# Kernel optimization log

Measured on AMD Instinct MI355X. Metric: run time of the kernel, lower is better.

Reference implementation:

```python
import jax, jax.numpy as jnp
import numpy as np

BSZ, L, D_Q, S_Q = 2, 2048, 512, 4
EPS = 1e-6


def quat_mul(a, b):
    ar, ai, aj, ak = a[..., 0], a[..., 1], a[..., 2], a[..., 3]
    br, bi, bj, bk = b[..., 0], b[..., 1], b[..., 2], b[..., 3]
    return jnp.stack((
        ar * br - ai * bi - aj * bj - ak * bk,
        ar * bi + ai * br + aj * bk - ak * bj,
        ar * bj - ai * bk + aj * br + ak * bi,
        ar * bk + ai * bj - aj * bi + ak * br,
    ), axis=-1)


def quat_inv(q):
    r, i, j, k = q[..., 0], q[..., 1], q[..., 2], q[..., 3]
    s = 1.0 / (r * r + i * i + j * j + k * k + EPS)
    return jnp.stack((r * s, -i * s, -j * s, -k * s), axis=-1)


def setup_inputs() -> dict:
    key = jax.random.key(0)
    ks = jax.random.split(key, 8)
    u = jax.random.normal(ks[0], (BSZ, L, D_Q, 4), dtype=jnp.float32)
    dt = jax.random.uniform(ks[1], (BSZ, L, D_Q), dtype=jnp.float32)
    B_in = jax.random.normal(ks[2], (BSZ, L, S_Q, 4), dtype=jnp.float32)
    C_in = jax.random.normal(ks[3], (BSZ, L, S_Q, 4), dtype=jnp.float32)
    # A_log init: log(arange(1, S_q+1)) repeated over D_q rows
    A_log = jnp.tile(jnp.log(jnp.arange(1, S_Q + 1, dtype=jnp.float32)), (D_Q, 1))
    A_i = jax.random.normal(ks[4], (D_Q, S_Q), dtype=jnp.float32) * 0.01
    A_j = jax.random.normal(ks[5], (D_Q, S_Q), dtype=jnp.float32) * 0.01
    A_k = jax.random.normal(ks[6], (D_Q, S_Q), dtype=jnp.float32) * 0.01
    return {"u": u, "dt": dt, "B_in": B_in, "C_in": C_in,
            "A_log": A_log, "A_i": A_i, "A_j": A_j, "A_k": A_k}


def reference(u, dt, B_in, C_in, A_log, A_i, A_j, A_k):
    # A quaternion: real part -exp(A_log), imaginary parts A_i/j/k  [D_q, S_q, 4]
    A_quat = jnp.stack([-jnp.exp(A_log), A_i, A_j, A_k], axis=-1)
    dt_b = dt[..., None, None]                      # [B, L, D_q, 1, 1]
    z = dt_b * A_quat                               # [B, L, D_q, S_q, 4]
    one = jnp.zeros_like(z).at[..., 0].set(1.0)     # quaternion identity
    num = one + 0.5 * z
    den = one - 0.5 * z
    den_inv = quat_inv(den)
    q = quat_mul(den_inv, num)                      # Cayley transition [B,L,D_q,S_q,4]
    dB = quat_mul(den_inv * dt_b, B_in[:, :, None])  # [B,L,D_q,S_q,4]
    Bu = quat_mul(dB, u[:, :, :, None])             # [B,L,D_q,S_q,4]

    def step(h, qb):
        qt, but = qb
        h = quat_mul(qt, h) + but
        return h, h

    h0 = jnp.zeros((u.shape[0], u.shape[2], A_quat.shape[1], 4), u.dtype)
    _, h_all = jax.lax.scan(step, h0, (jnp.swapaxes(q, 0, 1), jnp.swapaxes(Bu, 0, 1)))
    h_all = jnp.swapaxes(h_all, 0, 1)               # [B, L, D_q, S_q, 4]
    yh = quat_mul(C_in[:, :, None], h_all)
    return yh.sum(axis=3)                           # [B, L, D_q, 4]
```

## Files before the change

### kernel.cpp

```cpp
#include <hip/hip_runtime.h>

#define BSZ   2
#define LSEQ  2048
#define DQ    512
#define SQ    4
#define EPSQ  1e-6f

typedef float nfloat4 __attribute__((ext_vector_type(4)));
typedef float nfloat2 __attribute__((ext_vector_type(2)));

__device__ __forceinline__ nfloat2 mk2(float x, float y) { nfloat2 v; v.x = x; v.y = y; return v; }

struct PQuat { nfloat2 ri, jk; };

__device__ __forceinline__ PQuat pq_of(const float4 v) {
    PQuat p; p.ri = mk2(v.x, v.y); p.jk = mk2(v.z, v.w); return p;
}
__device__ __forceinline__ float4 f4_of(const PQuat p) {
    return make_float4(p.ri.x, p.ri.y, p.jk.x, p.jk.y);
}

__device__ __forceinline__ PQuat pqmul(const PQuat a, const PQuat b) {
    const float ar = a.ri.x, ai = a.ri.y, aj = a.jk.x, ak = a.jk.y;
    PQuat o;
    o.ri = ar*b.ri + ai*mk2(-b.ri.y,  b.ri.x)
         + aj*mk2(-b.jk.x,  b.jk.y) + ak*mk2(-b.jk.y, -b.jk.x);
    o.jk = ar*b.jk + ai*mk2(-b.jk.y,  b.jk.x)
         + aj*mk2( b.ri.x, -b.ri.y) + ak*mk2( b.ri.y,  b.ri.x);
    return o;
}

__device__ __forceinline__ PQuat pqmuladd(const PQuat a, const PQuat b, const PQuat c) {
    const float ar = a.ri.x, ai = a.ri.y, aj = a.jk.x, ak = a.jk.y;
    PQuat o;
    o.ri = c.ri + ar*b.ri + ai*mk2(-b.ri.y,  b.ri.x)
         + aj*mk2(-b.jk.x,  b.jk.y) + ak*mk2(-b.jk.y, -b.jk.x);
    o.jk = c.jk + ar*b.jk + ai*mk2(-b.jk.y,  b.jk.x)
         + aj*mk2( b.ri.x, -b.ri.y) + ak*mk2( b.ri.y,  b.ri.x);
    return o;
}

struct HA { float r, i; nfloat2 jk; float p2, n2r; };

__device__ __forceinline__ HA load_hA(const float* __restrict__ Alog,
                                      const float* __restrict__ Ai,
                                      const float* __restrict__ Aj,
                                      const float* __restrict__ Ak, int idx) {
    HA h;
    h.r  = -0.5f * __expf(Alog[idx]);
    h.i  =  0.5f * Ai[idx];
    h.jk = mk2(0.5f * Aj[idx], 0.5f * Ak[idx]);
    h.p2 = h.r*h.r + h.i*h.i + h.jk.x*h.jk.x + h.jk.y*h.jk.y;
    h.n2r = -2.0f * h.r;
    return h;
}

__device__ __forceinline__ void cayley_pk(const float a, const float aa, const HA& hA,
                                          const PQuat B, const PQuat U,
                                          PQuat& q, PQuat& Bu) {
    const float dd = __builtin_fmaf(aa, hA.p2, __builtin_fmaf(a, hA.n2r, 1.0f + EPSQ));
    const float sv = __builtin_amdgcn_rcpf(dd);
    const float nr = __builtin_fmaf(-aa, hA.p2, 1.0f);
    const float as = a * sv;
    const float s2a = as + as;
    q.ri = mk2(nr * sv, s2a * hA.i);
    q.jk = s2a * hA.jk;
    PQuat cd;
    cd.ri = mk2(__builtin_fmaf(-a, hA.r, 1.0f), a * hA.i);
    cd.jk = a * hA.jk;
    const PQuat cb = pqmul(cd, B);
    PQuat dB; dB.ri = as * cb.ri; dB.jk = as * cb.jk;
    Bu = pqmul(dB, U);
}

struct Quat { float r, i, j, k; };
__device__ __forceinline__ Quat qmul(const Quat a, const Quat b) {
    Quat o;
    o.r = a.r*b.r - a.i*b.i - a.j*b.j - a.k*b.k;
    o.i = a.r*b.i + a.i*b.r + a.j*b.k - a.k*b.j;
    o.j = a.r*b.j - a.i*b.k + a.j*b.r + a.k*b.i;
    o.k = a.r*b.k + a.i*b.j - a.j*b.i + a.k*b.r;
    return o;
}
__device__ __forceinline__ Quat qmuladd(const Quat a, const Quat b, const Quat c) {
    Quat o;
    o.r = c.r + a.r*b.r - a.i*b.i - a.j*b.j - a.k*b.k;
    o.i = c.i + a.r*b.i + a.i*b.r + a.j*b.k - a.k*b.j;
    o.j = c.j + a.r*b.j - a.i*b.k + a.j*b.r + a.k*b.i;
    o.k = c.k + a.r*b.k + a.i*b.j - a.j*b.i + a.k*b.r;
    return o;
}
__device__ __forceinline__ Quat q_of(const float4 v) { return Quat{v.x, v.y, v.z, v.w}; }
__device__ __forceinline__ float4 f4s_of(const Quat q) { return make_float4(q.r, q.i, q.j, q.k); }

template<int NCH>
__global__ __launch_bounds__(256, 6) void qssm_pass1(
    const float* __restrict__ u, const float* __restrict__ dt,
    const float* __restrict__ Bin,
    const float* __restrict__ Alog, const float* __restrict__ Ai,
    const float* __restrict__ Aj,   const float* __restrict__ Ak,
    float4* __restrict__ WQ, float4* __restrict__ WB)
{
    constexpr int CH = LSEQ / NCH;
    const int t  = threadIdx.x;
    const int dl = t & 127;
    const int sh = t >> 7;
    const int d  = blockIdx.x * 128 + dl;
    const int c  = blockIdx.y;
    const int b  = blockIdx.z;
    const int s0 = sh * 2;
    const int t0 = c * CH;

    HA hA[2];
    hA[0] = load_hA(Alog, Ai, Aj, Ak, d*SQ + s0);
    hA[1] = load_hA(Alog, Ai, Aj, Ak, d*SQ + s0 + 1);

    const int base = (b*LSEQ + t0);
    const float*  dtp = dt + (size_t)base*DQ + d;
    const float4* up  = (const float4*)u   + (size_t)base*DQ + d;
    const float4* Bp  = (const float4*)Bin + (size_t)base*SQ + s0;

    PQuat Q[2], Bc[2];
    {
        const float a  = *dtp;
        const float aa = a * a;
        const PQuat U  = pq_of(*up);
#pragma unroll
        for (int ss = 0; ss < 2; ++ss) {
            PQuat q, Bu;
            cayley_pk(a, aa, hA[ss], pq_of(Bp[ss]), U, q, Bu);
            Q[ss] = q; Bc[ss] = Bu;
        }
        dtp += DQ; up += DQ; Bp += SQ;
    }
#pragma unroll 2
    for (int j = 1; j < CH; ++j) {
        const float a  = *dtp;
        const float aa = a * a;
        const PQuat U  = pq_of(*up);
#pragma unroll
        for (int ss = 0; ss < 2; ++ss) {
            PQuat q, Bu;
            cayley_pk(a, aa, hA[ss], pq_of(Bp[ss]), U, q, Bu);
            Bc[ss] = pqmuladd(q, Bc[ss], Bu);
            Q[ss]  = pqmul(q, Q[ss]);
        }
        dtp += DQ; up += DQ; Bp += SQ;
    }
#pragma unroll
    for (int ss = 0; ss < 2; ++ss) {
        const size_t idx = ((size_t)(b*SQ + s0 + ss)*NCH + c)*DQ + d;
        WQ[idx] = f4_of(Q[ss]);
        WB[idx] = f4_of(Bc[ss]);
    }
}

template<int NCH>
__global__ __launch_bounds__(512) void qssm_pass2(
    const float4* __restrict__ WQ, float4* __restrict__ WB)
{
    constexpr int GS = 8;
    constexpr int NG = NCH / GS;
    __shared__ float4 QL[NG][16];
    __shared__ float4 BL[NG][16];
    __shared__ float4 HS[NG][16];

    const int t  = threadIdx.x;
    const int i  = t & 15;
    const int g  = t >> 4;
    const int bs = blockIdx.x >> 5;
    const int d  = (blockIdx.x & 31) * 16 + i;
    const size_t chbase = (size_t)bs * NCH * DQ + d;

    size_t idx = chbase + (size_t)(g * GS) * DQ;
    Quat Qa = q_of(WQ[idx]);
    Quat Ba = q_of(WB[idx]);
#pragma unroll
    for (int j = 1; j < GS; ++j) {
        idx += DQ;
        const Quat Qc = q_of(WQ[idx]);
        const Quat Bc = q_of(WB[idx]);
        Ba = qmuladd(Qc, Ba, Bc);
        Qa = qmul(Qc, Qa);
    }
    QL[g][i] = f4s_of(Qa);
    BL[g][i] = f4s_of(Ba);
    __syncthreads();

    if (t < 16) {
        Quat h{0.f, 0.f, 0.f, 0.f};
#pragma unroll
        for (int gg = 0; gg < NG; ++gg) {
            HS[gg][t] = f4s_of(h);
            h = qmuladd(q_of(QL[gg][t]), h, q_of(BL[gg][t]));
        }
    }
    __syncthreads();

    Quat h = q_of(HS[g][i]);
    idx = chbase + (size_t)(g * GS) * DQ;
#pragma unroll
    for (int j = 0; j < GS; ++j) {
        const Quat Qc = q_of(WQ[idx]);
        const Quat Bc = q_of(WB[idx]);
        WB[idx] = f4s_of(h);
        h = qmuladd(Qc, h, Bc);
        idx += DQ;
    }
}

template<int NCH>
__global__ __launch_bounds__(256, 6) void qssm_pass3(
    const float* __restrict__ u, const float* __restrict__ dt,
    const float* __restrict__ Bin, const float* __restrict__ Cin,
    const float* __restrict__ Alog, const float* __restrict__ Ai,
    const float* __restrict__ Aj,   const float* __restrict__ Ak,
    const float4* __restrict__ WB, float* __restrict__ out)
{
    constexpr int CH = LSEQ / NCH;
    const int t    = threadIdx.x;
    const int lane = t & 63;
    const int wv   = t >> 6;
    const int dl   = lane & 31;
    const int sh   = lane >> 5;
    const int s0   = sh * 2;
    const int d = blockIdx.x * 128 + wv * 32 + dl;
    const int c = blockIdx.y;
    const int b = blockIdx.z;
    const int t0 = c * CH;

    HA hA[2];
    PQuat h[2];
#pragma unroll
    for (int ss = 0; ss < 2; ++ss) {
        hA[ss] = load_hA(Alog, Ai, Aj, Ak, d*SQ + s0 + ss);
        h[ss] = pq_of(WB[((size_t)(b*SQ + s0 + ss)*NCH + c)*DQ + d]);
    }
    const int base = (b*LSEQ + t0);
    const float*  dtp  = dt + (size_t)base*DQ + d;
    const float4* up   = (const float4*)u   + (size_t)base*DQ + d;
    const float4* Bp   = (const float4*)Bin + (size_t)base*SQ + s0;
    const float4* Cp   = (const float4*)Cin + (size_t)base*SQ + s0;
    nfloat4*      outp = (nfloat4*)out + (size_t)base*DQ + d;

#pragma unroll 2
    for (int j = 0; j < CH; ++j) {
        const float a  = *dtp;
        const float aa = a * a;
        const PQuat U  = pq_of(*up);
        PQuat y; y.ri = mk2(0.f, 0.f); y.jk = mk2(0.f, 0.f);
#pragma unroll
        for (int ss = 0; ss < 2; ++ss) {
            const PQuat Cq = pq_of(Cp[ss]);
            PQuat q, Bu;
            cayley_pk(a, aa, hA[ss], pq_of(Bp[ss]), U, q, Bu);
            h[ss] = pqmuladd(q, h[ss], Bu);
            y = pqmuladd(Cq, h[ss], y);
        }
        float yr = y.ri.x + __shfl_xor(y.ri.x, 32);
        float yi = y.ri.y + __shfl_xor(y.ri.y, 32);
        float yj = y.jk.x + __shfl_xor(y.jk.x, 32);
        float yk = y.jk.y + __shfl_xor(y.jk.y, 32);
        if (sh == 0) {
            const nfloat4 yv = {yr, yi, yj, yk};
            __builtin_nontemporal_store(yv, outp);
        }
        dtp += DQ; up += DQ; Bp += SQ; Cp += SQ; outp += DQ;
    }
}

template<int NCH>
static void launch_all(const float* u, const float* dt, const float* Bin,
                       const float* Cin, const float* Alog, const float* Ai,
                       const float* Aj, const float* Ak,
                       float* out, void* d_ws, hipStream_t stream) {
    const size_t elems = (size_t)BSZ * SQ * NCH * DQ;
    float4* WQ = (float4*)d_ws;
    float4* WB = WQ + elems;
    dim3 g1(DQ / 128, NCH, BSZ);
    qssm_pass1<NCH><<<g1, 256, 0, stream>>>(u, dt, Bin, Alog, Ai, Aj, Ak, WQ, WB);
    qssm_pass2<NCH><<<(BSZ*SQ*DQ)/16, 16*(NCH/8), 0, stream>>>(WQ, WB);
    dim3 g3(DQ / 128, NCH, BSZ);
    qssm_pass3<NCH><<<g3, 256, 0, stream>>>(u, dt, Bin, Cin, Alog, Ai, Aj, Ak, WB, out);
}

extern "C" void kernel_launch(void* const* d_in, const int* in_sizes, int n_in,
                              void* d_out, int out_size, void* d_ws, size_t ws_size,
                              hipStream_t stream) {
    const float* u    = (const float*)d_in[0];
    const float* dt   = (const float*)d_in[1];
    const float* Bin  = (const float*)d_in[2];
    const float* Cin  = (const float*)d_in[3];
    const float* Alog = (const float*)d_in[4];
    const float* Ai   = (const float*)d_in[5];
    const float* Aj   = (const float*)d_in[6];
    const float* Ak   = (const float*)d_in[7];
    float* out = (float*)d_out;

    auto ws_need = [](int nch) -> size_t {
        return 2ull * BSZ * SQ * (size_t)nch * DQ * sizeof(float4);
    };
    if (ws_size >= ws_need(256)) {
        launch_all<256>(u, dt, Bin, Cin, Alog, Ai, Aj, Ak, out, d_ws, stream);
    } else if (ws_size >= ws_need(128)) {
        launch_all<128>(u, dt, Bin, Cin, Alog, Ai, Aj, Ak, out, d_ws, stream);
    } else {
        launch_all<64>(u, dt, Bin, Cin, Alog, Ai, Aj, Ak, out, d_ws, stream);
    }
}
```

Before: 156.1 us.

## Fuse three scan passes into one cooperative kernel with grid syncs

```diff
diff --git a/kernel.cpp b/kernel.cpp
--- a/kernel.cpp
+++ b/kernel.cpp
@@ -1,4 +1,7 @@
 #include <hip/hip_runtime.h>
+#include <hip/hip_cooperative_groups.h>
+
+namespace cg = cooperative_groups;
 
 #define BSZ   2
 #define LSEQ  2048
@@ -92,6 +95,188 @@
 }
 __device__ __forceinline__ Quat q_of(const float4 v) { return Quat{v.x, v.y, v.z, v.w}; }
 __device__ __forceinline__ float4 f4s_of(const Quat q) { return make_float4(q.r, q.i, q.j, q.k); }
+
+template<int NCH>
+__global__ __launch_bounds__(256, 4) void qssm_fused(
+    const float* __restrict__ u, const float* __restrict__ dt,
+    const float* __restrict__ Bin, const float* __restrict__ Cin,
+    const float* __restrict__ Alog, const float* __restrict__ Ai,
+    const float* __restrict__ Aj,   const float* __restrict__ Ak,
+    float4* __restrict__ WQ, float4* __restrict__ WB, float* __restrict__ out)
+{
+    constexpr int CH  = LSEQ / NCH;
+    constexpr int NDB = DQ / 128;
+    constexpr int NT  = BSZ * NCH * NDB;
+    constexpr int NUNITS = (BSZ * SQ) * (DQ / 16);
+    constexpr int GS  = NCH / 16;
+
+    __shared__ float4 QL[16][16];
+    __shared__ float4 BL[16][16];
+    __shared__ float4 HS[16][16];
+
+    const int t = threadIdx.x;
+    cg::grid_group grid = cg::this_grid();
+
+    {
+        const int dl = t & 127;
+        const int sh = t >> 7;
+        const int s0 = sh * 2;
+        for (int tid = blockIdx.x; tid < NT; tid += gridDim.x) {
+            const int dblk = tid % NDB;
+            const int c    = (tid / NDB) % NCH;
+            const int b    =  tid / (NDB * NCH);
+            const int d    = dblk * 128 + dl;
+            const int t0   = c * CH;
+
+            HA hA0 = load_hA(Alog, Ai, Aj, Ak, d*SQ + s0);
+            HA hA1 = load_hA(Alog, Ai, Aj, Ak, d*SQ + s0 + 1);
+
+            const int base = (b*LSEQ + t0);
+            const float*  dtp = dt + (size_t)base*DQ + d;
+            const float4* up  = (const float4*)u   + (size_t)base*DQ + d;
+            const float4* Bp  = (const float4*)Bin + (size_t)base*SQ + s0;
+
+            PQuat Q[2], Bc[2];
+            {
+                const float a  = *dtp;
+                const float aa = a * a;
+                const PQuat U  = pq_of(*up);
+                PQuat q, Bu;
+                cayley_pk(a, aa, hA0, pq_of(Bp[0]), U, q, Bu);
+                Q[0] = q; Bc[0] = Bu;
+                cayley_pk(a, aa, hA1, pq_of(Bp[1]), U, q, Bu);
+                Q[1] = q; Bc[1] = Bu;
+                dtp += DQ; up += DQ; Bp += SQ;
+            }
+#pragma unroll 2
+            for (int j = 1; j < CH; ++j) {
+                const float a  = *dtp;
+                const float aa = a * a;
+                const PQuat U  = pq_of(*up);
+                PQuat q, Bu;
+                cayley_pk(a, aa, hA0, pq_of(Bp[0]), U, q, Bu);
+                Bc[0] = pqmuladd(q, Bc[0], Bu);
+                Q[0]  = pqmul(q, Q[0]);
+                cayley_pk(a, aa, hA1, pq_of(Bp[1]), U, q, Bu);
+                Bc[1] = pqmuladd(q, Bc[1], Bu);
+                Q[1]  = pqmul(q, Q[1]);
+                dtp += DQ; up += DQ; Bp += SQ;
+            }
+#pragma unroll
+            for (int ss = 0; ss < 2; ++ss) {
+                const size_t idx = ((size_t)(b*SQ + s0 + ss)*NCH + c)*DQ + d;
+                WQ[idx] = f4_of(Q[ss]);
+                WB[idx] = f4_of(Bc[ss]);
+            }
+        }
+    }
+    grid.sync();
+
+    if (blockIdx.x < NUNITS) {
+        const int i  = t & 15;
+        const int g  = t >> 4;
+        const int bs = blockIdx.x >> 5;
+        const int d  = (blockIdx.x & 31) * 16 + i;
+        const size_t chbase = (size_t)bs * NCH * DQ + d;
+
+        Quat Qa{1.f, 0.f, 0.f, 0.f};
+        Quat Ba{0.f, 0.f, 0.f, 0.f};
+        size_t idx0 = chbase + (size_t)(g * GS) * DQ;
+        for (int j0 = 0; j0 < GS; j0 += 4) {
+            float4 qv[4], bv[4];
+#pragma unroll
+            for (int j = 0; j < 4; ++j) {
+                qv[j] = WQ[idx0 + (size_t)(j0 + j) * DQ];
+                bv[j] = WB[idx0 + (size_t)(j0 + j) * DQ];
+            }
+#pragma unroll
+            for (int j = 0; j < 4; ++j) {
+                Ba = qmuladd(q_of(qv[j]), Ba, q_of(bv[j]));
+                Qa = qmul(q_of(qv[j]), Qa);
+            }
+        }
+        QL[g][i] = f4s_of(Qa);
+        BL[g][i] = f4s_of(Ba);
+        __syncthreads();
+
+        if (t < 16) {
+            Quat h{0.f, 0.f, 0.f, 0.f};
+#pragma unroll
+            for (int gg = 0; gg < 16; ++gg) {
+                HS[gg][t] = f4s_of(h);
+                h = qmuladd(q_of(QL[gg][t]), h, q_of(BL[gg][t]));
+            }
+        }
+        __syncthreads();
+
+        Quat h = q_of(HS[g][i]);
+        for (int j0 = 0; j0 < GS; j0 += 4) {
+            float4 qv[4], bv[4];
+#pragma unroll
+            for (int j = 0; j < 4; ++j) {
+                qv[j] = WQ[idx0 + (size_t)(j0 + j) * DQ];
+                bv[j] = WB[idx0 + (size_t)(j0 + j) * DQ];
+            }
+#pragma unroll
+            for (int j = 0; j < 4; ++j) {
+                WB[idx0 + (size_t)(j0 + j) * DQ] = f4s_of(h);
+                h = qmuladd(q_of(qv[j]), h, q_of(bv[j]));
+            }
+        }
+    }
+    grid.sync();
+
+    {
+        const int lane = t & 63;
+        const int wv   = t >> 6;
+        const int dl   = lane & 31;
+        const int sh   = lane >> 5;
+        const int s0   = sh * 2;
+        for (int tid = blockIdx.x; tid < NT; tid += gridDim.x) {
+            const int dblk = tid % NDB;
+            const int c    = (tid / NDB) % NCH;
+            const int b    =  tid / (NDB * NCH);
+            const int d    = dblk * 128 + wv * 32 + dl;
+            const int t0   = c * CH;
+
+            HA hA0 = load_hA(Alog, Ai, Aj, Ak, d*SQ + s0);
+            HA hA1 = load_hA(Alog, Ai, Aj, Ak, d*SQ + s0 + 1);
+            PQuat h0 = pq_of(WB[((size_t)(b*SQ + s0    )*NCH + c)*DQ + d]);
+            PQuat h1 = pq_of(WB[((size_t)(b*SQ + s0 + 1)*NCH + c)*DQ + d]);
+
+            const int base = (b*LSEQ + t0);
+            const float*  dtp  = dt + (size_t)base*DQ + d;
+            const float4* up   = (const float4*)u   + (size_t)base*DQ + d;
+            const float4* Bp   = (const float4*)Bin + (size_t)base*SQ + s0;
+            const float4* Cp   = (const float4*)Cin + (size_t)base*SQ + s0;
+            nfloat4*      outp = (nfloat4*)out + (size_t)base*DQ + d;
+
+#pragma unroll 2
+            for (int j = 0; j < CH; ++j) {
+                const float a  = *dtp;
+                const float aa = a * a;
+                const PQuat U  = pq_of(*up);
+                PQuat y; y.ri = mk2(0.f, 0.f); y.jk = mk2(0.f, 0.f);
+                PQuat q, Bu;
+                cayley_pk(a, aa, hA0, pq_of(Bp[0]), U, q, Bu);
+                h0 = pqmuladd(q, h0, Bu);
+                y  = pqmuladd(pq_of(Cp[0]), h0, y);
+                cayley_pk(a, aa, hA1, pq_of(Bp[1]), U, q, Bu);
+                h1 = pqmuladd(q, h1, Bu);
+                y  = pqmuladd(pq_of(Cp[1]), h1, y);
+                float yr = y.ri.x + __shfl_xor(y.ri.x, 32);
+                float yi = y.ri.y + __shfl_xor(y.ri.y, 32);
+                float yj = y.jk.x + __shfl_xor(y.jk.x, 32);
+                float yk = y.jk.y + __shfl_xor(y.jk.y, 32);
+                if (sh == 0) {
+                    const nfloat4 yv = {yr, yi, yj, yk};
+                    __builtin_nontemporal_store(yv, outp);
+                }
+                dtp += DQ; up += DQ; Bp += SQ; Cp += SQ; outp += DQ;
+            }
+        }
+    }
+}
 
 template<int NCH>
 __global__ __launch_bounds__(256, 6) void qssm_pass1(
@@ -277,6 +462,16 @@
     const size_t elems = (size_t)BSZ * SQ * NCH * DQ;
     float4* WQ = (float4*)d_ws;
     float4* WB = WQ + elems;
+
+    void* kargs[] = {(void*)&u, (void*)&dt, (void*)&Bin, (void*)&Cin,
+                     (void*)&Alog, (void*)&Ai, (void*)&Aj, (void*)&Ak,
+                     (void*)&WQ, (void*)&WB, (void*)&out};
+    hipError_t e = hipLaunchCooperativeKernel(
+        reinterpret_cast<void*>(qssm_fused<NCH>),
+        dim3(1024), dim3(256), kargs, 0, stream);
+    if (e == hipSuccess) return;
+    (void)hipGetLastError();
+
     dim3 g1(DQ / 128, NCH, BSZ);
     qssm_pass1<NCH><<<g1, 256, 0, stream>>>(u, dt, Bin, Alog, Ai, Aj, Ak, WQ, WB);
     qssm_pass2<NCH><<<(BSZ*SQ*DQ)/16, 16*(NCH/8), 0, stream>>>(WQ, WB);
```

Result: slower. 407.7 us (+161.2%).

## Stage per-chunk u, dt, B, C tiles into LDS via async global_load_lds

Applied to the files above, without the earlier changes.

```diff
diff --git a/kernel.cpp b/kernel.cpp
--- a/kernel.cpp
+++ b/kernel.cpp
@@ -93,6 +93,18 @@
 __device__ __forceinline__ Quat q_of(const float4 v) { return Quat{v.x, v.y, v.z, v.w}; }
 __device__ __forceinline__ float4 f4s_of(const Quat q) { return make_float4(q.r, q.i, q.j, q.k); }
 
+typedef unsigned int u32_t;
+__device__ __forceinline__ void gl_lds16(const void* g, void* l) {
+    __builtin_amdgcn_global_load_lds(
+        (const __attribute__((address_space(1))) u32_t*)g,
+        (__attribute__((address_space(3))) u32_t*)l, 16, 0, 0);
+}
+__device__ __forceinline__ void gl_lds4(const void* g, void* l) {
+    __builtin_amdgcn_global_load_lds(
+        (const __attribute__((address_space(1))) u32_t*)g,
+        (__attribute__((address_space(3))) u32_t*)l, 4, 0, 0);
+}
+
 template<int NCH>
 __global__ __launch_bounds__(256, 6) void qssm_pass1(
     const float* __restrict__ u, const float* __restrict__ dt,
@@ -102,50 +114,70 @@
     float4* __restrict__ WQ, float4* __restrict__ WB)
 {
     constexpr int CH = LSEQ / NCH;
-    const int t  = threadIdx.x;
+    __shared__ float4 uL[CH][128];
+    __shared__ float  dtL[CH][128];
+    __shared__ float4 BL[CH][SQ];
+
+    const int t    = threadIdx.x;
+    const int lane = t & 63;
+    const int wid  = t >> 6;
+    const int dblk = blockIdx.x;
+    const int c    = blockIdx.y;
+    const int b    = blockIdx.z;
+    const int t0   = c * CH;
+    const int base = b*LSEQ + t0;
+
+    const float4* ug  = (const float4*)u + (size_t)base*DQ + dblk*128;
+    const float*  dtg = dt + (size_t)base*DQ + dblk*128;
+    const float*  Bg  = Bin + (size_t)base*SQ*4;
+#pragma unroll
+    for (int jj = 0; jj < CH/4; ++jj) {
+        const int j = wid*(CH/4) + jj;
+#pragma unroll
+        for (int k = 0; k < 2; ++k) {
+            gl_lds16(ug  + (size_t)j*DQ + k*64 + lane, &uL[j][k*64]);
+            gl_lds4 (dtg + (size_t)j*DQ + k*64 + lane, &dtL[j][k*64]);
+        }
+    }
+    if (wid == 0) {
+#pragma unroll
+        for (int k = 0; k < 2; ++k)
+            gl_lds4(Bg + k*64 + lane, ((float*)BL) + k*64);
+    }
+
     const int dl = t & 127;
     const int sh = t >> 7;
-    const int d  = blockIdx.x * 128 + dl;
-    const int c  = blockIdx.y;
-    const int b  = blockIdx.z;
     const int s0 = sh * 2;
-    const int t0 = c * CH;
-
-    HA hA[2];
-    hA[0] = load_hA(Alog, Ai, Aj, Ak, d*SQ + s0);
-    hA[1] = load_hA(Alog, Ai, Aj, Ak, d*SQ + s0 + 1);
-
-    const int base = (b*LSEQ + t0);
-    const float*  dtp = dt + (size_t)base*DQ + d;
-    const float4* up  = (const float4*)u   + (size_t)base*DQ + d;
-    const float4* Bp  = (const float4*)Bin + (size_t)base*SQ + s0;
+    const int d  = dblk*128 + dl;
+
+    HA hA0 = load_hA(Alog, Ai, Aj, Ak, d*SQ + s0);
+    HA hA1 = load_hA(Alog, Ai, Aj, Ak, d*SQ + s0 + 1);
+
+    __syncthreads();
 
     PQuat Q[2], Bc[2];
     {
-        const float a  = *dtp;
+        const float a  = dtL[0][dl];
         const float aa = a * a;
-        const PQuat U  = pq_of(*up);
-#pragma unroll
-        for (int ss = 0; ss < 2; ++ss) {
-            PQuat q, Bu;
-            cayley_pk(a, aa, hA[ss], pq_of(Bp[ss]), U, q, Bu);
-            Q[ss] = q; Bc[ss] = Bu;
-        }
-        dtp += DQ; up += DQ; Bp += SQ;
-    }
-#pragma unroll 2
+        const PQuat U  = pq_of(uL[0][dl]);
+        PQuat q, Bu;
+        cayley_pk(a, aa, hA0, pq_of(BL[0][s0]),     U, q, Bu);
+        Q[0] = q; Bc[0] = Bu;
+        cayley_pk(a, aa, hA1, pq_of(BL[0][s0 + 1]), U, q, Bu);
+        Q[1] = q; Bc[1] = Bu;
+    }
+#pragma unroll
     for (int j = 1; j < CH; ++j) {
-        const float a  = *dtp;
+        const float a  = dtL[j][dl];
         const float aa = a * a;
-        const PQuat U  = pq_of(*up);
-#pragma unroll
-        for (int ss = 0; ss < 2; ++ss) {
-            PQuat q, Bu;
-            cayley_pk(a, aa, hA[ss], pq_of(Bp[ss]), U, q, Bu);
-            Bc[ss] = pqmuladd(q, Bc[ss], Bu);
-            Q[ss]  = pqmul(q, Q[ss]);
-        }
-        dtp += DQ; up += DQ; Bp += SQ;
+        const PQuat U  = pq_of(uL[j][dl]);
+        PQuat q, Bu;
+        cayley_pk(a, aa, hA0, pq_of(BL[j][s0]),     U, q, Bu);
+        Bc[0] = pqmuladd(q, Bc[0], Bu);
+        Q[0]  = pqmul(q, Q[0]);
+        cayley_pk(a, aa, hA1, pq_of(BL[j][s0 + 1]), U, q, Bu);
+        Bc[1] = pqmuladd(q, Bc[1], Bu);
+        Q[1]  = pqmul(q, Q[1]);
     }
 #pragma unroll
     for (int ss = 0; ss < 2; ++ss) {
@@ -162,7 +194,7 @@
     constexpr int GS = 8;
     constexpr int NG = NCH / GS;
     __shared__ float4 QL[NG][16];
-    __shared__ float4 BL[NG][16];
+    __shared__ float4 BL2[NG][16];
     __shared__ float4 HS[NG][16];
 
     const int t  = threadIdx.x;
@@ -183,8 +215,8 @@
         Ba = qmuladd(Qc, Ba, Bc);
         Qa = qmul(Qc, Qa);
     }
-    QL[g][i] = f4s_of(Qa);
-    BL[g][i] = f4s_of(Ba);
+    QL[g][i]  = f4s_of(Qa);
+    BL2[g][i] = f4s_of(Ba);
     __syncthreads();
 
     if (t < 16) {
@@ -192,7 +224,7 @@
 #pragma unroll
         for (int gg = 0; gg < NG; ++gg) {
             HS[gg][t] = f4s_of(h);
-            h = qmuladd(q_of(QL[gg][t]), h, q_of(BL[gg][t]));
+            h = qmuladd(q_of(QL[gg][t]), h, q_of(BL2[gg][t]));
         }
     }
     __syncthreads();
@@ -218,45 +250,71 @@
     const float4* __restrict__ WB, float* __restrict__ out)
 {
     constexpr int CH = LSEQ / NCH;
+    __shared__ float4 uL[CH][128];
+    __shared__ float  dtL[CH][128];
+    __shared__ float4 BL[CH][SQ];
+    __shared__ float4 CL[CH][SQ];
+
     const int t    = threadIdx.x;
     const int lane = t & 63;
-    const int wv   = t >> 6;
-    const int dl   = lane & 31;
-    const int sh   = lane >> 5;
-    const int s0   = sh * 2;
-    const int d = blockIdx.x * 128 + wv * 32 + dl;
-    const int c = blockIdx.y;
-    const int b = blockIdx.z;
-    const int t0 = c * CH;
-
-    HA hA[2];
-    PQuat h[2];
-#pragma unroll
-    for (int ss = 0; ss < 2; ++ss) {
-        hA[ss] = load_hA(Alog, Ai, Aj, Ak, d*SQ + s0 + ss);
-        h[ss] = pq_of(WB[((size_t)(b*SQ + s0 + ss)*NCH + c)*DQ + d]);
-    }
-    const int base = (b*LSEQ + t0);
-    const float*  dtp  = dt + (size_t)base*DQ + d;
-    const float4* up   = (const float4*)u   + (size_t)base*DQ + d;
-    const float4* Bp   = (const float4*)Bin + (size_t)base*SQ + s0;
-    const float4* Cp   = (const float4*)Cin + (size_t)base*SQ + s0;
-    nfloat4*      outp = (nfloat4*)out + (size_t)base*DQ + d;
-
-#pragma unroll 2
+    const int wid  = t >> 6;
+    const int dblk = blockIdx.x;
+    const int c    = blockIdx.y;
+    const int b    = blockIdx.z;
+    const int t0   = c * CH;
+    const int base = b*LSEQ + t0;
+
+    const float4* ug  = (const float4*)u + (size_t)base*DQ + dblk*128;
+    const float*  dtg = dt + (size_t)base*DQ + dblk*128;
+    const float*  Bg  = Bin + (size_t)base*SQ*4;
+    const float*  Cg  = Cin + (size_t)base*SQ*4;
+#pragma unroll
+    for (int jj = 0; jj < CH/4; ++jj) {
+        const int j = wid*(CH/4) + jj;
+#pragma unroll
+        for (int k = 0; k < 2; ++k) {
+            gl_lds16(ug  + (size_t)j*DQ + k*64 + lane, &uL[j][k*64]);
+            gl_lds4 (dtg + (size_t)j*DQ + k*64 + lane, &dtL[j][k*64]);
+        }
+    }
+    if (wid == 0) {
+#pragma unroll
+        for (int k = 0; k < 2; ++k)
+            gl_lds4(Bg + k*64 + lane, ((float*)BL) + k*64);
+    } else if (wid == 1) {
+#pragma unroll
+        for (int k = 0; k < 2; ++k)
+            gl_lds4(Cg + k*64 + lane, ((float*)CL) + k*64);
+    }
+
+    const int dl = lane & 31;
+    const int sh = lane >> 5;
+    const int s0 = sh * 2;
+    const int dloc = wid*32 + dl;
+    const int d    = dblk*128 + dloc;
+
+    HA hA0 = load_hA(Alog, Ai, Aj, Ak, d*SQ + s0);
+    HA hA1 = load_hA(Alog, Ai, Aj, Ak, d*SQ + s0 + 1);
+    PQuat h0 = pq_of(WB[((size_t)(b*SQ + s0    )*NCH + c)*DQ + d]);
+    PQuat h1 = pq_of(WB[((size_t)(b*SQ + s0 + 1)*NCH + c)*DQ + d]);
+
+    nfloat4* outp = (nfloat4*)out + (size_t)base*DQ + d;
+
+    __syncthreads();
+
+#pragma unroll
     for (int j = 0; j < CH; ++j) {
-        const float a  = *dtp;
+        const float a  = dtL[j][dloc];
         const float aa = a * a;
-        const PQuat U  = pq_of(*up);
+        const PQuat U  = pq_of(uL[j][dloc]);
         PQuat y; y.ri = mk2(0.f, 0.f); y.jk = mk2(0.f, 0.f);
-#pragma unroll
-        for (int ss = 0; ss < 2; ++ss) {
-            const PQuat Cq = pq_of(Cp[ss]);
-            PQuat q, Bu;
-            cayley_pk(a, aa, hA[ss], pq_of(Bp[ss]), U, q, Bu);
-            h[ss] = pqmuladd(q, h[ss], Bu);
-            y = pqmuladd(Cq, h[ss], y);
-        }
+        PQuat q, Bu;
+        cayley_pk(a, aa, hA0, pq_of(BL[j][s0]),     U, q, Bu);
+        h0 = pqmuladd(q, h0, Bu);
+        y  = pqmuladd(pq_of(CL[j][s0]),     h0, y);
+        cayley_pk(a, aa, hA1, pq_of(BL[j][s0 + 1]), U, q, Bu);
+        h1 = pqmuladd(q, h1, Bu);
+        y  = pqmuladd(pq_of(CL[j][s0 + 1]), h1, y);
         float yr = y.ri.x + __shfl_xor(y.ri.x, 32);
         float yi = y.ri.y + __shfl_xor(y.ri.y, 32);
         float yj = y.jk.x + __shfl_xor(y.jk.x, 32);
@@ -265,7 +323,7 @@
             const nfloat4 yv = {yr, yi, yj, yk};
             __builtin_nontemporal_store(yv, outp);
         }
-        dtp += DQ; up += DQ; Bp += SQ; Cp += SQ; outp += DQ;
+        outp += DQ;
     }
 }
 
```

Result: faster. 151.7 us (-2.8%).
